# Optimization experiments

Measured on AMD Instinct MI355X. Metric: run time of the kernel, lower is better.

Reference implementation:

```python
import jax, jax.numpy as jnp
import numpy as np

DIM = 256
NUM_HEADS = 8
HEAD_DIM = DIM // NUM_HEADS
SCALE = 1.0 / DIM ** 0.5  # NOTE: source scales by 1/sqrt(dim), not 1/sqrt(head_dim)


def setup_inputs() -> dict:
    key = jax.random.key(0)
    k_x, k_wqkv, k_wout = jax.random.split(key, 3)
    x = jax.random.normal(k_x, (4, 2048, DIM), dtype=jnp.float32)
    # xavier_uniform for Linear(dim, 3*dim): limit = sqrt(6/(fan_in+fan_out))
    lim_qkv = float(np.sqrt(6.0 / (DIM + 3 * DIM)))
    w_qkv = jax.random.uniform(k_wqkv, (3 * DIM, DIM), minval=-lim_qkv, maxval=lim_qkv, dtype=jnp.float32)
    b_qkv = jnp.zeros((3 * DIM,), dtype=jnp.float32)
    lim_out = float(np.sqrt(6.0 / (DIM + DIM)))
    w_out = jax.random.uniform(k_wout, (DIM, DIM), minval=-lim_out, maxval=lim_out, dtype=jnp.float32)
    b_out = jnp.zeros((DIM,), dtype=jnp.float32)
    return {"x": x, "w_qkv": w_qkv, "b_qkv": b_qkv, "w_out": w_out, "b_out": b_out}


def reference(x, w_qkv, b_qkv, w_out, b_out):
    B, N, C = x.shape
    H, D = NUM_HEADS, C // NUM_HEADS
    qkv = x @ w_qkv.T + b_qkv                       # [B, N, 3C]
    qkv = qkv.reshape(B, N, 3, H, D)
    q = qkv[:, :, 0].transpose(0, 2, 1, 3)          # [B, H, N, D]
    k = qkv[:, :, 1].transpose(0, 2, 1, 3)
    v = qkv[:, :, 2].transpose(0, 2, 1, 3)
    attn = jnp.einsum("bhnd,bhmd->bhnm", q, k) * SCALE  # [B, H, N, N]
    attn = jax.nn.softmax(attn, axis=-1)
    z = jnp.einsum("bhnm,bhmd->bhnd", attn, v)      # [B, H, N, D]
    z = z.transpose(0, 2, 1, 3).reshape(B, N, C)
    return z @ w_out.T + b_out
```

## Files before the change

kernel.cpp:

```cpp
#include <hip/hip_runtime.h>


#define SEQ 2048
#define BATCH 4
#define NHEADS 8
#define HDIM 32
#define DIMC 256
#define SCALE_LOG2E 0.09016844005556021f

typedef __attribute__((ext_vector_type(8))) short short8;
typedef __attribute__((ext_vector_type(4))) float f32x4;

union BF8 { unsigned u[4]; short8 s8; };

__device__ __forceinline__ unsigned pk2bf(float a, float b) {
    union { float f; unsigned u; } ua, ub;
    ua.f = a; ub.f = b;
    return __builtin_amdgcn_perm(ub.u + 0x8000u, ua.u + 0x8000u, 0x07060302u);
}
__device__ __forceinline__ short f2bf(float a) {
    union { float f; unsigned u; } x; x.f = a;
    return (short)((x.u + 0x8000u) >> 16);
}

#define NX (BATCH * SEQ * DIMC)
#define NQW (3 * DIMC * DIMC)
#define NOW (DIMC * DIMC)

__global__ __launch_bounds__(256) void cvt_bf16(const float* __restrict__ x,
                                                const float* __restrict__ wq,
                                                const float* __restrict__ wo,
                                                short* __restrict__ xb,
                                                short* __restrict__ wqb,
                                                short* __restrict__ wob) {
    int i = (blockIdx.x * 256 + threadIdx.x) * 4;
    const float* src;
    short* dst;
    int off;
    if (i < NX) { src = x; dst = xb; off = i; }
    else if (i < NX + NQW) { src = wq; dst = wqb; off = i - NX; }
    else { src = wo; dst = wob; off = i - NX - NQW; }
    float4 v = *(const float4*)&src[off];
    uint2 p;
    p.x = pk2bf(v.x, v.y);
    p.y = pk2bf(v.z, v.w);
    *(uint2*)&dst[off] = p;
}

__global__ __launch_bounds__(256) void qkv_mfma(const short* __restrict__ Xb,
                                                const short* __restrict__ Wb,
                                                const float* __restrict__ bias,
                                                short* __restrict__ Q,
                                                short* __restrict__ Kd,
                                                short* __restrict__ V) {
    __shared__ __align__(16) union SM {
        struct { short A[128][72]; short B[64][72]; } ab;
        short CQ[128][72];
        short CV[64][136];
    } sm;

    const int m0 = blockIdx.y * 128, bx = blockIdx.x;
    const int n0 = bx * 64;
    const int tid = threadIdx.x;
    const int w = tid >> 6, lane = tid & 63;
    const int m = lane & 15, g = lane >> 4;
    const int wr = w >> 1, wc = w & 1;

    const int arow = tid >> 1, acol = (tid & 1) * 32;
    const int brow = tid >> 2, bcol = (tid & 3) * 16;

    f32x4 acc[4][2] = {};

    const short* ap = Xb + (size_t)(m0 + arow) * DIMC + acol;
    const short* bp = Wb + (size_t)(n0 + brow) * DIMC + bcol;

    short8 pa[4], pb[2];
#pragma unroll
    for (int i = 0; i < 4; i++) pa[i] = *(const short8*)(ap + i * 8);
#pragma unroll
    for (int i = 0; i < 2; i++) pb[i] = *(const short8*)(bp + i * 8);

    for (int kt = 0; kt < DIMC; kt += 64) {
        __syncthreads();
#pragma unroll
        for (int i = 0; i < 4; i++) *(short8*)&sm.ab.A[arow][acol + i * 8] = pa[i];
#pragma unroll
        for (int i = 0; i < 2; i++) *(short8*)&sm.ab.B[brow][bcol + i * 8] = pb[i];
        __syncthreads();
        if (kt + 64 < DIMC) {
#pragma unroll
            for (int i = 0; i < 4; i++) pa[i] = *(const short8*)(ap + kt + 64 + i * 8);
#pragma unroll
            for (int i = 0; i < 2; i++) pb[i] = *(const short8*)(bp + kt + 64 + i * 8);
        }
#pragma unroll
        for (int kk = 0; kk < 2; kk++) {
            short8 af[4], bf[2];
#pragma unroll
            for (int mt = 0; mt < 4; mt++)
                af[mt] = *(const short8*)&sm.ab.A[wr * 64 + mt * 16 + m][kk * 32 + g * 8];
#pragma unroll
            for (int nt = 0; nt < 2; nt++)
                bf[nt] = *(const short8*)&sm.ab.B[wc * 32 + nt * 16 + m][kk * 32 + g * 8];
#pragma unroll
            for (int mt = 0; mt < 4; mt++)
#pragma unroll
                for (int nt = 0; nt < 2; nt++)
                    acc[mt][nt] = __builtin_amdgcn_mfma_f32_16x16x32_bf16(af[mt], bf[nt], acc[mt][nt], 0, 0, 0);
        }
    }

    const int which = bx >> 2;
    const int h0 = (bx & 3) * 2;
    const int bidx = blockIdx.y >> 4;
    const int ntok0 = (blockIdx.y & 15) * 128;
    float bv[2];
#pragma unroll
    for (int nt = 0; nt < 2; nt++) bv[nt] = bias[n0 + wc * 32 + nt * 16 + m];

    __syncthreads();
    if (which != 2) {
        const float qs = (which == 0) ? SCALE_LOG2E : 1.0f;
#pragma unroll
        for (int mt = 0; mt < 4; mt++)
#pragma unroll
            for (int nt = 0; nt < 2; nt++)
#pragma unroll
                for (int r = 0; r < 4; r++)
                    sm.CQ[wr * 64 + mt * 16 + g * 4 + r][wc * 32 + nt * 16 + m] =
                        f2bf((acc[mt][nt][r] + bv[nt]) * qs);
        __syncthreads();
        short* dst = (which == 0) ? Q : Kd;
        const int tok = tid >> 1, d0 = (tid & 1) * 16;
#pragma unroll
        for (int hh = 0; hh < 2; hh++) {
            size_t o = ((size_t)((bidx * NHEADS + h0 + hh) * SEQ) + ntok0 + tok) * HDIM + d0;
            *(short8*)&dst[o] = *(const short8*)&sm.CQ[tok][hh * 32 + d0];
            *(short8*)&dst[o + 8] = *(const short8*)&sm.CQ[tok][hh * 32 + d0 + 8];
        }
    } else {
#pragma unroll
        for (int mt = 0; mt < 4; mt++)
#pragma unroll
            for (int nt = 0; nt < 2; nt++) {
                uint2 p;
                p.x = pk2bf(acc[mt][nt][0] + bv[nt], acc[mt][nt][1] + bv[nt]);
                p.y = pk2bf(acc[mt][nt][2] + bv[nt], acc[mt][nt][3] + bv[nt]);
                *(uint2*)&sm.CV[wc * 32 + nt * 16 + m][wr * 64 + mt * 16 + g * 4] = p;
            }
        __syncthreads();
        const int col = tid >> 2, t0 = (tid & 3) * 32;
        const int hh = col >> 5, d = col & 31;
        size_t o = ((size_t)((bidx * NHEADS + h0 + hh) * HDIM) + d) * SEQ + ntok0 + t0;
#pragma unroll
        for (int c2 = 0; c2 < 4; c2++)
            *(short8*)&V[o + c2 * 8] = *(const short8*)&sm.CV[col][t0 + c2 * 8];
    }
}

__global__ __launch_bounds__(256) void attn_tile(const short* __restrict__ Q,
                                                 const short* __restrict__ K,
                                                 const short* __restrict__ V,
                                                 short* __restrict__ Zb) {
    __shared__ __align__(16) union SM {
        struct { short Ks[2][128][40]; short Vs[2][32][136]; } kv;
        struct { float O[4][64][36]; float L[4][64]; } ep;
    } sm;

    const int bh = blockIdx.y;
    const int b = bh >> 3, h = bh & 7;
    const int q0 = blockIdx.x * 64;
    const short* qb = Q + (size_t)bh * SEQ * HDIM;
    const short* kb = K + (size_t)bh * SEQ * HDIM;
    const short* vb = V + (size_t)bh * HDIM * SEQ;
    const int tid = threadIdx.x;
    const int w = tid >> 6, lane = tid & 63;
    const int m = lane & 15, g = lane >> 4;

    short8 qfr[4];
#pragma unroll
    for (int qt = 0; qt < 4; qt++)
        qfr[qt] = *(const short8*)(qb + (size_t)(q0 + qt * 16 + m) * HDIM + g * 8);

    const int krow = tid >> 1, kcol = (tid & 1) * 16;
    const int rl = krow & 31;
    const int lrow = (krow & ~31) | (((rl >> 2) & 1) << 4) | ((rl >> 3) << 2) | (rl & 3);
    const int vrow = tid >> 3, vcol = (tid & 7) * 16;

    f32x4 o[4][2] = {};
    f32x4 ol[4] = {};
    const short8 ones = {0x3F80, 0x3F80, 0x3F80, 0x3F80, 0x3F80, 0x3F80, 0x3F80, 0x3F80};

    short8 k0a = *(const short8*)(kb + (size_t)krow * HDIM + kcol);
    short8 k0b = *(const short8*)(kb + (size_t)krow * HDIM + kcol + 8);
    short8 v0a = *(const short8*)(vb + (size_t)vrow * SEQ + vcol);
    short8 v0b = *(const short8*)(vb + (size_t)vrow * SEQ + vcol + 8);
    *(short8*)&sm.kv.Ks[0][lrow][kcol] = k0a;
    *(short8*)&sm.kv.Ks[0][lrow][kcol + 8] = k0b;
    *(short8*)&sm.kv.Vs[0][vrow][vcol] = v0a;
    *(short8*)&sm.kv.Vs[0][vrow][vcol + 8] = v0b;
    __syncthreads();

    for (int it = 0; it < SEQ / 128; ++it) {
        const int buf = it & 1;
        if (it < SEQ / 128 - 1) {
            const int kn = (it + 1) * 128;
            k0a = *(const short8*)(kb + (size_t)(kn + krow) * HDIM + kcol);
            k0b = *(const short8*)(kb + (size_t)(kn + krow) * HDIM + kcol + 8);
            v0a = *(const short8*)(vb + (size_t)vrow * SEQ + kn + vcol);
            v0b = *(const short8*)(vb + (size_t)vrow * SEQ + kn + vcol + 8);
        }

        short8 kf0 = *(const short8*)&sm.kv.Ks[buf][w * 32 + m][g * 8];
        short8 kf1 = *(const short8*)&sm.kv.Ks[buf][w * 32 + 16 + m][g * 8];
        short8 vf0 = *(const short8*)&sm.kv.Vs[buf][m][w * 32 + g * 8];
        short8 vf1 = *(const short8*)&sm.kv.Vs[buf][16 + m][w * 32 + g * 8];

#pragma unroll
        for (int qt = 0; qt < 4; qt++) {
            f32x4 z4 = {0.f, 0.f, 0.f, 0.f};
            f32x4 st0 = __builtin_amdgcn_mfma_f32_16x16x32_bf16(kf0, qfr[qt], z4, 0, 0, 0);
            f32x4 st1 = __builtin_amdgcn_mfma_f32_16x16x32_bf16(kf1, qfr[qt], z4, 0, 0, 0);
            BF8 a;
            a.u[0] = pk2bf(__builtin_amdgcn_exp2f(st0[0]), __builtin_amdgcn_exp2f(st0[1]));
            a.u[1] = pk2bf(__builtin_amdgcn_exp2f(st0[2]), __builtin_amdgcn_exp2f(st0[3]));
            a.u[2] = pk2bf(__builtin_amdgcn_exp2f(st1[0]), __builtin_amdgcn_exp2f(st1[1]));
            a.u[3] = pk2bf(__builtin_amdgcn_exp2f(st1[2]), __builtin_amdgcn_exp2f(st1[3]));
            o[qt][0] = __builtin_amdgcn_mfma_f32_16x16x32_bf16(a.s8, vf0, o[qt][0], 0, 0, 0);
            o[qt][1] = __builtin_amdgcn_mfma_f32_16x16x32_bf16(a.s8, vf1, o[qt][1], 0, 0, 0);
            ol[qt] = __builtin_amdgcn_mfma_f32_16x16x32_bf16(a.s8, ones, ol[qt], 0, 0, 0);
        }

        if (it < SEQ / 128 - 1) {
            const int nb = buf ^ 1;
            *(short8*)&sm.kv.Ks[nb][lrow][kcol] = k0a;
            *(short8*)&sm.kv.Ks[nb][lrow][kcol + 8] = k0b;
            *(short8*)&sm.kv.Vs[nb][vrow][vcol] = v0a;
            *(short8*)&sm.kv.Vs[nb][vrow][vcol + 8] = v0b;
        }
        __syncthreads();
    }

#pragma unroll
    for (int qt = 0; qt < 4; qt++) {
#pragma unroll
        for (int dh = 0; dh < 2; dh++)
#pragma unroll
            for (int r = 0; r < 4; r++)
                sm.ep.O[w][qt * 16 + g * 4 + r][dh * 16 + m] = o[qt][dh][r];
        if (m == 0)
#pragma unroll
            for (int r = 0; r < 4; r++)
                sm.ep.L[w][qt * 16 + g * 4 + r] = ol[qt][r];
    }
    __syncthreads();

    const int ql = tid >> 2, d0 = (tid & 3) * 8;
    float lt = sm.ep.L[0][ql] + sm.ep.L[1][ql] + sm.ep.L[2][ql] + sm.ep.L[3][ql];
    float inv = __builtin_amdgcn_rcpf(lt);
    float sv[8];
#pragma unroll
    for (int j = 0; j < 8; j++)
        sv[j] = sm.ep.O[0][ql][d0 + j] + sm.ep.O[1][ql][d0 + j] +
                sm.ep.O[2][ql][d0 + j] + sm.ep.O[3][ql][d0 + j];
    BF8 pz;
#pragma unroll
    for (int j = 0; j < 4; j++)
        pz.u[j] = pk2bf(sv[2 * j] * inv, sv[2 * j + 1] * inv);
    *(short8*)&Zb[(size_t)(b * SEQ + q0 + ql) * DIMC + h * HDIM + d0] = pz.s8;
}

__global__ __launch_bounds__(256) void out_mfma(const short* __restrict__ A,
                                                const short* __restrict__ Wb,
                                                const float* __restrict__ bias,
                                                float* __restrict__ C) {
    __shared__ __align__(16) short As[64][72];
    __shared__ __align__(16) short Bs[64][72];
    const int m0 = blockIdx.y * 64, n0 = blockIdx.x * 64;
    const int tid = threadIdx.x;
    const int w = tid >> 6, lane = tid & 63;
    const int m = lane & 15, g = lane >> 4;
    const int srow = tid >> 2, scol = (tid & 3) * 16;

    f32x4 acc[4] = {};

    const short* ap = A + (size_t)(m0 + srow) * DIMC + scol;
    const short* bp = Wb + (size_t)(n0 + srow) * DIMC + scol;

    short8 pa[2], pb[2];
#pragma unroll
    for (int i = 0; i < 2; i++) {
        pa[i] = *(const short8*)(ap + i * 8);
        pb[i] = *(const short8*)(bp + i * 8);
    }

    for (int kt = 0; kt < DIMC; kt += 64) {
        __syncthreads();
#pragma unroll
        for (int i = 0; i < 2; i++) {
            *(short8*)&As[srow][scol + i * 8] = pa[i];
            *(short8*)&Bs[srow][scol + i * 8] = pb[i];
        }
        __syncthreads();
        if (kt + 64 < DIMC) {
#pragma unroll
            for (int i = 0; i < 2; i++) {
                pa[i] = *(const short8*)(ap + kt + 64 + i * 8);
                pb[i] = *(const short8*)(bp + kt + 64 + i * 8);
            }
        }
#pragma unroll
        for (int kk = 0; kk < 2; kk++) {
            short8 af = *(const short8*)&As[w * 16 + m][kk * 32 + g * 8];
#pragma unroll
            for (int nt = 0; nt < 4; nt++) {
                short8 bf = *(const short8*)&Bs[nt * 16 + m][kk * 32 + g * 8];
                acc[nt] = __builtin_amdgcn_mfma_f32_16x16x32_bf16(af, bf, acc[nt], 0, 0, 0);
            }
        }
    }

    float bv[4];
#pragma unroll
    for (int nt = 0; nt < 4; nt++) bv[nt] = bias[n0 + nt * 16 + m];
#pragma unroll
    for (int nt = 0; nt < 4; nt++)
#pragma unroll
        for (int r = 0; r < 4; r++)
            C[(size_t)(m0 + w * 16 + g * 4 + r) * DIMC + n0 + nt * 16 + m] = acc[nt][r] + bv[nt];
}

extern "C" void kernel_launch(void* const* d_in, const int* in_sizes, int n_in,
                              void* d_out, int out_size, void* d_ws, size_t ws_size,
                              hipStream_t stream) {
    const float* x     = (const float*)d_in[0];
    const float* w_qkv = (const float*)d_in[1];
    const float* b_qkv = (const float*)d_in[2];
    const float* w_out = (const float*)d_in[3];
    const float* b_out = (const float*)d_in[4];
    float* out = (float*)d_out;

    const size_t HSZ = (size_t)BATCH * NHEADS * SEQ * HDIM;
    short* xb  = (short*)d_ws;
    short* wqb = xb + NX;
    short* wob = wqb + NQW;
    short* qw  = wob + NOW;
    short* kw  = qw + HSZ;
    short* vw  = kw + HSZ;
    short* zb  = vw + HSZ;

    cvt_bf16<<<(NX + NQW + NOW) / 1024, 256, 0, stream>>>(x, w_qkv, w_out, xb, wqb, wob);
    qkv_mfma<<<dim3(12, 64), 256, 0, stream>>>(xb, wqb, b_qkv, qw, kw, vw);
    attn_tile<<<dim3(32, 32), 256, 0, stream>>>(qw, kw, vw, zb);
    out_mfma<<<dim3(4, 128), 256, 0, stream>>>(zb, wob, b_out, out);
}
```

Before: 120.0 us.

## Share K/V tiles across two query halves with 512-thread attention blocks

The attention kernel now processes 128 queries per block using 512 threads. Each K/V 128-key tile loaded into shared memory serves two groups of 64 query rows instead of one, which halves global K/V reads and LDS staging per query. Each thread now loads one short8 per tile instead of two. The epilogue reduction buffer doubles to cover 128 rows. The risks are fewer blocks in the grid, a larger LDS footprint, and register pressure from the launch_bounds(512,4) hint.

Measured after the change: 112.8 us. 1.06x faster.

```diff
diff --git a/kernel.cpp b/kernel.cpp
--- a/kernel.cpp
+++ b/kernel.cpp
@@ -158,63 +158,58 @@
     }
 }
 
-__global__ __launch_bounds__(256) void attn_tile(const short* __restrict__ Q,
-                                                 const short* __restrict__ K,
-                                                 const short* __restrict__ V,
-                                                 short* __restrict__ Zb) {
+__global__ __launch_bounds__(512, 4) void attn_tile(const short* __restrict__ Q,
+                                                    const short* __restrict__ K,
+                                                    const short* __restrict__ V,
+                                                    short* __restrict__ Zb) {
     __shared__ __align__(16) union SM {
         struct { short Ks[2][128][40]; short Vs[2][32][136]; } kv;
-        struct { float O[4][64][36]; float L[4][64]; } ep;
+        struct { float O[4][128][36]; float L[4][128]; } ep;
     } sm;
 
     const int bh = blockIdx.y;
     const int b = bh >> 3, h = bh & 7;
-    const int q0 = blockIdx.x * 64;
+    const int q0 = blockIdx.x * 128;
     const short* qb = Q + (size_t)bh * SEQ * HDIM;
     const short* kb = K + (size_t)bh * SEQ * HDIM;
     const short* vb = V + (size_t)bh * HDIM * SEQ;
     const int tid = threadIdx.x;
     const int w = tid >> 6, lane = tid & 63;
     const int m = lane & 15, g = lane >> 4;
+    const int ks = w & 3, qh = w >> 2;
 
     short8 qfr[4];
 #pragma unroll
     for (int qt = 0; qt < 4; qt++)
-        qfr[qt] = *(const short8*)(qb + (size_t)(q0 + qt * 16 + m) * HDIM + g * 8);
-
-    const int krow = tid >> 1, kcol = (tid & 1) * 16;
+        qfr[qt] = *(const short8*)(qb + (size_t)(q0 + qh * 64 + qt * 16 + m) * HDIM + g * 8);
+
+    const int krow = tid >> 2, kcol = (tid & 3) * 8;
     const int rl = krow & 31;
     const int lrow = (krow & ~31) | (((rl >> 2) & 1) << 4) | ((rl >> 3) << 2) | (rl & 3);
-    const int vrow = tid >> 3, vcol = (tid & 7) * 16;
+    const int vrow = tid >> 4, vcol = (tid & 15) * 8;
 
     f32x4 o[4][2] = {};
     f32x4 ol[4] = {};
     const short8 ones = {0x3F80, 0x3F80, 0x3F80, 0x3F80, 0x3F80, 0x3F80, 0x3F80, 0x3F80};
 
-    short8 k0a = *(const short8*)(kb + (size_t)krow * HDIM + kcol);
-    short8 k0b = *(const short8*)(kb + (size_t)krow * HDIM + kcol + 8);
-    short8 v0a = *(const short8*)(vb + (size_t)vrow * SEQ + vcol);
-    short8 v0b = *(const short8*)(vb + (size_t)vrow * SEQ + vcol + 8);
-    *(short8*)&sm.kv.Ks[0][lrow][kcol] = k0a;
-    *(short8*)&sm.kv.Ks[0][lrow][kcol + 8] = k0b;
-    *(short8*)&sm.kv.Vs[0][vrow][vcol] = v0a;
-    *(short8*)&sm.kv.Vs[0][vrow][vcol + 8] = v0b;
+    short8 k0 = *(const short8*)(kb + (size_t)krow * HDIM + kcol);
+    short8 v0 = *(const short8*)(vb + (size_t)vrow * SEQ + vcol);
+    *(short8*)&sm.kv.Ks[0][lrow][kcol] = k0;
+    *(short8*)&sm.kv.Vs[0][vrow][vcol] = v0;
     __syncthreads();
 
     for (int it = 0; it < SEQ / 128; ++it) {
         const int buf = it & 1;
         if (it < SEQ / 128 - 1) {
             const int kn = (it + 1) * 128;
-            k0a = *(const short8*)(kb + (size_t)(kn + krow) * HDIM + kcol);
-            k0b = *(const short8*)(kb + (size_t)(kn + krow) * HDIM + kcol + 8);
-            v0a = *(const short8*)(vb + (size_t)vrow * SEQ + kn + vcol);
-            v0b = *(const short8*)(vb + (size_t)vrow * SEQ + kn + vcol + 8);
-        }
-
-        short8 kf0 = *(const short8*)&sm.kv.Ks[buf][w * 32 + m][g * 8];
-        short8 kf1 = *(const short8*)&sm.kv.Ks[buf][w * 32 + 16 + m][g * 8];
-        short8 vf0 = *(const short8*)&sm.kv.Vs[buf][m][w * 32 + g * 8];
-        short8 vf1 = *(const short8*)&sm.kv.Vs[buf][16 + m][w * 32 + g * 8];
+            k0 = *(const short8*)(kb + (size_t)(kn + krow) * HDIM + kcol);
+            v0 = *(const short8*)(vb + (size_t)vrow * SEQ + kn + vcol);
+        }
+
+        short8 kf0 = *(const short8*)&sm.kv.Ks[buf][ks * 32 + m][g * 8];
+        short8 kf1 = *(const short8*)&sm.kv.Ks[buf][ks * 32 + 16 + m][g * 8];
+        short8 vf0 = *(const short8*)&sm.kv.Vs[buf][m][ks * 32 + g * 8];
+        short8 vf1 = *(const short8*)&sm.kv.Vs[buf][16 + m][ks * 32 + g * 8];
 
 #pragma unroll
         for (int qt = 0; qt < 4; qt++) {
@@ -233,25 +228,24 @@
 
         if (it < SEQ / 128 - 1) {
             const int nb = buf ^ 1;
-            *(short8*)&sm.kv.Ks[nb][lrow][kcol] = k0a;
-            *(short8*)&sm.kv.Ks[nb][lrow][kcol + 8] = k0b;
-            *(short8*)&sm.kv.Vs[nb][vrow][vcol] = v0a;
-            *(short8*)&sm.kv.Vs[nb][vrow][vcol + 8] = v0b;
+            *(short8*)&sm.kv.Ks[nb][lrow][kcol] = k0;
+            *(short8*)&sm.kv.Vs[nb][vrow][vcol] = v0;
         }
         __syncthreads();
     }
 
 #pragma unroll
     for (int qt = 0; qt < 4; qt++) {
+        const int row = qh * 64 + qt * 16 + g * 4;
 #pragma unroll
         for (int dh = 0; dh < 2; dh++)
 #pragma unroll
             for (int r = 0; r < 4; r++)
-                sm.ep.O[w][qt * 16 + g * 4 + r][dh * 16 + m] = o[qt][dh][r];
+                sm.ep.O[ks][row + r][dh * 16 + m] = o[qt][dh][r];
         if (m == 0)
 #pragma unroll
             for (int r = 0; r < 4; r++)
-                sm.ep.L[w][qt * 16 + g * 4 + r] = ol[qt][r];
+                sm.ep.L[ks][row + r] = ol[qt][r];
     }
     __syncthreads();
 
@@ -351,6 +345,6 @@
 
     cvt_bf16<<<(NX + NQW + NOW) / 1024, 256, 0, stream>>>(x, w_qkv, w_out, xb, wqb, wob);
     qkv_mfma<<<dim3(12, 64), 256, 0, stream>>>(xb, wqb, b_qkv, qw, kw, vw);
-    attn_tile<<<dim3(32, 32), 256, 0, stream>>>(qw, kw, vw, zb);
+    attn_tile<<<dim3(16, 32), 512, 0, stream>>>(qw, kw, vw, zb);
     out_mfma<<<dim3(4, 128), 256, 0, stream>>>(zb, wob, b_out, out);
 }
```
